# Kernel tuning notes

Hardware: AMD Instinct MI355X
Metric: run time of the kernel (lower is better)

Reference implementation:

```python
import jax, jax.numpy as jnp
from jax import lax
import numpy as np
import math

A = 9          # anchors per location
NC = 80        # classes
SCORE_T = 0.05
NMS_T = 0.5
DPI = 100      # detections_per_img (also per-level K in _inference)
BBOX_CLIP = math.log(1000.0 / 16.0)
LEVEL_SHAPES = [(64, 64), (32, 32), (16, 16), (8, 8)]
STRIDES = [8, 16, 32, 64]
BASE_SIZES = [32, 64, 128, 256]


def _conv(x, w, b):
    y = lax.conv_general_dilated(x, w, (1, 1), 'SAME', dimension_numbers=('NCHW', 'OIHW', 'NCHW'))
    return y + b[None, :, None, None]


def _head(feats, tower_w, tower_b, out_w, out_b, out_dim):
    outs = []
    for f in feats:
        x = f
        for i in range(tower_w.shape[0]):
            x = jax.nn.relu(_conv(x, tower_w[i], tower_b[i]))
        x = _conv(x, out_w, out_b)                     # [B, A*out_dim, H, W]
        B, _, H, W = x.shape
        x = x.reshape(B, A, out_dim, H, W).transpose(0, 3, 4, 1, 2).reshape(B, H * W * A, out_dim)
        outs.append(x)
    return outs


def _clip_boxes(b, img_h, img_w):
    x1 = jnp.clip(b[:, 0], 0.0, float(img_w)); y1 = jnp.clip(b[:, 1], 0.0, float(img_h))
    x2 = jnp.clip(b[:, 2], 0.0, float(img_w)); y2 = jnp.clip(b[:, 3], 0.0, float(img_h))
    return jnp.stack([x1, y1, x2, y2], axis=-1)


def _level_anchors(H, W, stride, s, img_h, img_w):
    # torchvision AnchorGenerator: sizes (s, s*2^(1/3), s*2^(2/3)), ratios (0.5,1,2)
    sizes = jnp.array([s, int(s * 2 ** (1 / 3)), int(s * 2 ** (2 / 3))], dtype=jnp.float32)
    ratios = jnp.array([0.5, 1.0, 2.0], dtype=jnp.float32)
    h_r = jnp.sqrt(ratios); w_r = 1.0 / h_r
    ws = (w_r[:, None] * sizes[None, :]).reshape(-1)
    hs = (h_r[:, None] * sizes[None, :]).reshape(-1)
    base = jnp.round(jnp.stack([-ws, -hs, ws, hs], axis=-1) / 2.0)   # [9,4]
    sx = (jnp.arange(W) * stride).astype(jnp.float32)
    sy = (jnp.arange(H) * stride).astype(jnp.float32)
    yy, xx = jnp.meshgrid(sy, sx, indexing='ij')
    shifts = jnp.stack([xx, yy, xx, yy], axis=-1).reshape(-1, 1, 4)   # [H*W,1,4]
    anch = (shifts + base[None]).reshape(-1, 4)                        # [H*W*A,4]
    return _clip_boxes(anch, img_h, img_w)


def _decode(rel, anch):
    # BoxCoder.decode_single with weights (1,1,1,1)
    w = anch[:, 2] - anch[:, 0]; h = anch[:, 3] - anch[:, 1]
    cx = anch[:, 0] + 0.5 * w;   cy = anch[:, 1] + 0.5 * h
    dx, dy = rel[:, 0], rel[:, 1]
    dw = jnp.minimum(rel[:, 2], BBOX_CLIP)
    dh = jnp.minimum(rel[:, 3], BBOX_CLIP)
    pcx = dx * w + cx; pcy = dy * h + cy
    pw = jnp.exp(dw) * w; ph = jnp.exp(dh) * h
    return jnp.stack([pcx - 0.5 * pw, pcy - 0.5 * ph, pcx + 0.5 * pw, pcy + 0.5 * ph], axis=-1)


def _pairwise_iou(boxes):
    area = (boxes[:, 2] - boxes[:, 0]) * (boxes[:, 3] - boxes[:, 1])
    lt = jnp.maximum(boxes[:, None, :2], boxes[None, :, :2])
    rb = jnp.minimum(boxes[:, None, 2:], boxes[None, :, 2:])
    wh = jnp.clip(rb - lt, 0.0)
    inter = wh[..., 0] * wh[..., 1]
    return inter / (area[:, None] + area[None, :] - inter + 1e-9)


def _per_image(logits, regs, anchors, img_h, img_w):
    bs, ss, ls = [], [], []
    for logit, reg, anch in zip(logits, regs, anchors):
        scores = jax.nn.sigmoid(logit).reshape(-1)                   # [N*NC]
        masked = jnp.where(scores > SCORE_T, scores, -1.0)
        top_s, idx = lax.top_k(masked, DPI)                          # fixed K = detections_per_img
        aidx = idx // NC
        lbl = idx % NC
        boxes = _clip_boxes(_decode(reg[aidx], anch[aidx]), img_h, img_w)
        valid = top_s > SCORE_T
        bs.append(boxes)
        ss.append(jnp.where(valid, top_s, -1.0))
        ls.append(jnp.where(valid, lbl, -1))
    boxes = jnp.concatenate(bs, 0); scores = jnp.concatenate(ss, 0); labels = jnp.concatenate(ls, 0)
    # batched (per-class) NMS via label coordinate offsets
    order = jnp.argsort(-scores)
    boxes_s = boxes[order]; scores_s = scores[order]; labels_s = labels[order]
    offset = labels_s.astype(boxes.dtype) * (float(max(img_h, img_w)) + 1.0)
    iou = lax.stop_gradient(_pairwise_iou(boxes_s + offset[:, None]))
    N = scores_s.shape[0]
    ar = jnp.arange(N)
    def body(i, keep):
        sup = keep[i] & (iou[i] > NMS_T) & (ar > i)
        return keep & ~sup
    keep = lax.fori_loop(0, N, body, scores_s > SCORE_T)
    fs, fi = lax.top_k(jnp.where(keep, scores_s, -1.0), DPI)
    ok = fs > SCORE_T
    fb = jnp.where(ok[:, None], boxes_s[fi], 0.0)
    fl = jnp.where(ok, labels_s[fi], -1)
    fs = jnp.where(ok, fs, 0.0)
    return fb, fs, fl


def setup_inputs() -> dict:
    key = jax.random.key(0)
    ks = jax.random.split(key, 8)
    B = 4
    w_scale = 0.04
    inp = {}
    shapes = [(B, 256, 64, 64), (B, 256, 32, 32), (B, 256, 16, 16), (B, 256, 8, 8)]
    for i, sh in enumerate(shapes):
        inp[f'f{i}'] = jax.random.normal(ks[i], sh, dtype=jnp.float32)
    inp['cls_tower_w'] = jax.random.normal(ks[4], (4, 256, 256, 3, 3), dtype=jnp.float32) * w_scale
    inp['cls_tower_b'] = jnp.zeros((4, 256), dtype=jnp.float32)
    inp['cls_out_w'] = jax.random.normal(ks[5], (A * NC, 256, 3, 3), dtype=jnp.float32) * w_scale
    inp['cls_out_b'] = jnp.full((A * NC,), -2.0, dtype=jnp.float32)  # prior-like bias
    inp['reg_tower_w'] = jax.random.normal(ks[6], (4, 256, 256, 3, 3), dtype=jnp.float32) * w_scale
    inp['reg_tower_b'] = jnp.zeros((4, 256), dtype=jnp.float32)
    inp['reg_out_w'] = jax.random.normal(ks[7], (A * 4, 256, 3, 3), dtype=jnp.float32) * w_scale
    inp['reg_out_b'] = jnp.zeros((A * 4,), dtype=jnp.float32)
    inp['image_h'] = 512
    inp['image_w'] = 512
    return inp


def reference(f0, f1, f2, f3, cls_tower_w, cls_tower_b, cls_out_w, cls_out_b,
              reg_tower_w, reg_tower_b, reg_out_w, reg_out_b, image_h, image_w):
    feats = [f0, f1, f2, f3]
    cls_logits = _head(feats, cls_tower_w, cls_tower_b, cls_out_w, cls_out_b, NC)   # list of [B,Ni,NC]
    bbox_regs = _head(feats, reg_tower_w, reg_tower_b, reg_out_w, reg_out_b, 4)     # list of [B,Ni,4]
    anchors = [_level_anchors(H, W, st, s, image_h, image_w)
               for (H, W), st, s in zip(LEVEL_SHAPES, STRIDES, BASE_SIZES)]
    fn = lambda ls, rs: _per_image(ls, rs, anchors, image_h, image_w)
    boxes, scores, labels = jax.vmap(fn)(tuple(cls_logits), tuple(bbox_regs))
    return boxes, scores, labels
```

## Files before the change

kernel.cpp:

```cpp
#include <hip/hip_runtime.h>
#include <math.h>

#define A_NUM 9
#define NCLS 80
#define IMG_KEY 3916800
#define IMG_REG 195840
#define CAP 8192
#define HBINS 16384

#define PCHUNK 12032
#define CHUNK_SLOTS 24064
#define CHUNK_BYTES (CHUNK_SLOTS * 16)
#define ACT_SLAB ((size_t)CHUNK_BYTES * 16)
#define WCHUNK_BYTES 40960
#define WCOG_BYTES (WCHUNK_BYTES * 16)

typedef _Float16 h8 __attribute__((ext_vector_type(8)));
typedef float fx4 __attribute__((ext_vector_type(4)));
typedef unsigned short u16;

__constant__ int   c_W[4]       = {64, 32, 16, 8};
__constant__ int   c_stride[4]  = {8, 16, 32, 64};
__constant__ float c_sizes[4][3]= {{32.f,40.f,50.f},{64.f,80.f,101.f},{128.f,161.f,203.f},{256.f,322.f,406.f}};
__constant__ int   c_keyOff[4]  = {0, 2949120, 3686400, 3870720};
__constant__ int   c_keyCnt[4]  = {2949120, 737280, 184320, 46080};
__constant__ int   c_regOff[4]  = {0, 147456, 184320, 193536};
__constant__ int   c_C[4]       = {66, 34, 18, 18};
__constant__ int   c_plvl[4]    = {0, 8712, 11024, 11672};
__constant__ int   c_pOff[4]    = {0, 1024, 1280, 1344};

__device__ __forceinline__ void gl_lds16(const void* g, void* l) {
    __builtin_amdgcn_global_load_lds(
        (const __attribute__((address_space(1))) void*)g,
        (__attribute__((address_space(3))) void*)l, 16, 0, 0);
}

__global__ __launch_bounds__(256) void pad16_k(
    const float* __restrict__ f0, const float* __restrict__ f1,
    const float* __restrict__ f2, const float* __restrict__ f3,
    char* __restrict__ Pin)
{
    int idx = blockIdx.x * 256 + threadIdx.x;
    const int PER_IMG = 16 * 2 * 1360;
    if (idx >= 4 * PER_IMG) return;
    int img = idx / PER_IMG;
    int r = idx - img * PER_IMG;
    int chunk = r / (2 * 1360);
    int r2 = r - chunk * (2 * 1360);
    int hfsel = r2 / 1360;
    int p = r2 - hfsel * 1360;
    int lvl = (p < 1024) ? 0 : (p < 1280 ? 1 : (p < 1344 ? 2 : 3));
    int u = p - c_pOff[lvl];
    int sh = 4 - lvl;
    int y = u >> sh;
    int xg = u & ((1 << sh) - 1);
    int x0 = xg * 4;
    int W = 64 >> lvl;
    const float* f = (lvl == 0) ? f0 : (lvl == 1) ? f1 : (lvl == 2) ? f2 : f3;
    int ci0 = chunk * 16 + hfsel * 8;
    float4 v[8];
    #pragma unroll
    for (int j = 0; j < 8; ++j)
        v[j] = *reinterpret_cast<const float4*>(
            f + ((size_t)(img * 256 + ci0 + j)) * (W * W) + y * W + x0);
    char* base = Pin + (size_t)img * ACT_SLAB + (size_t)chunk * CHUNK_BYTES;
    const int C = c_C[lvl];
    size_t rowSlot = (size_t)c_plvl[lvl] + (size_t)((y + 1) * 2 + hfsel) * C;
    #pragma unroll
    for (int c = 0; c < 4; ++c) {
        h8 hv, lv;
        #pragma unroll
        for (int j = 0; j < 8; ++j) {
            float val = (c == 0) ? v[j].x : (c == 1) ? v[j].y : (c == 2) ? v[j].z : v[j].w;
            _Float16 hh = (_Float16)val;
            hv[j] = hh;
            lv[j] = (_Float16)(val - (float)hh);
        }
        size_t slot = rowSlot + (x0 + c + 1);
        *reinterpret_cast<h8*>(base + slot * 16) = hv;
        *reinterpret_cast<h8*>(base + (slot + PCHUNK) * 16) = lv;
    }
}

__global__ __launch_bounds__(256) void repack16_k(
    const float* __restrict__ src, u16* __restrict__ dst,
    int C_out, int nCg, int total)
{
    int idx = blockIdx.x * 256 + threadIdx.x;
    if (idx >= total) return;
    int per = nCg * 16 * 1280;
    int layer = idx / per;
    int r = idx - layer * per;
    int cg = r / (16 * 1280);
    int r2 = r - cg * (16 * 1280);
    int chunk = r2 / 1280;
    int s = r2 - chunk * 1280;
    int co = s & 63;
    int r3 = s >> 6;
    int hfsel = r3 & 1;
    int kk = r3 >> 1;
    int coG = cg * 64 + co;
    float v[8];
    if (kk < 9 && coG < C_out) {
        const float* sp = src + ((size_t)(layer * C_out + coG)) * 2304
                        + (size_t)(chunk * 16 + hfsel * 8) * 9 + kk;
        #pragma unroll
        for (int j = 0; j < 8; ++j) v[j] = sp[j * 9];
    } else {
        #pragma unroll
        for (int j = 0; j < 8; ++j) v[j] = 0.f;
    }
    h8 hv, lv;
    #pragma unroll
    for (int j = 0; j < 8; ++j) {
        _Float16 hh = (_Float16)v[j];
        hv[j] = hh;
        lv[j] = (_Float16)(v[j] - (float)hh);
    }
    size_t e = ((size_t)((layer * nCg + cg) * 16 + chunk)) * 20480
             + (size_t)(kk >> 1) * 2048 + (size_t)(kk & 1) * 1024
             + (size_t)hfsel * 512 + (size_t)co * 8;
    *reinterpret_cast<h8*>(dst + e) = hv;
    *reinterpret_cast<h8*>(dst + e + 10240) = lv;
}

__global__ __launch_bounds__(256, 2) void conv16(
    const char* __restrict__ Pin, const char* __restrict__ bufIn, char* __restrict__ bufOut,
    const u16* __restrict__ repA, const float* __restrict__ bA,
    const u16* __restrict__ repB, const float* __restrict__ bB,
    unsigned* __restrict__ keys, float* __restrict__ regb,
    int mode, int usePin)
{
    const int tid = threadIdx.x;
    const int lane = tid & 63;
    const int wv = tid >> 6;

    int img, head, coBase, C_out, epi, tile;
    if (mode == 0) {
        int hw = blockIdx.x;
        int logical = (hw & 7) * 88 + (hw >> 3);
        int z = logical / 88;
        int rem = logical - z * 88;
        tile = rem >> 2;
        coBase = (rem & 3) * 64;
        img = z & 3; head = z >> 2;
        C_out = 256; epi = 0;
    } else {
        int hw = blockIdx.x;
        int logical = (hw & 7) * 143 + (hw >> 3);
        img = logical / 286;
        int rem = logical - img * 286;
        tile = rem / 13;
        int yy = rem - tile * 13;
        if (yy < 12) { head = 0; coBase = yy * 64; C_out = 720; epi = 1; }
        else         { head = 1; coBase = 0;       C_out = 36;  epi = 2; }
    }
    const float* bsel = head ? bB : bA;
    const u16* wsel = head ? repB : repA;
    const char* wBase = (const char*)wsel + (size_t)(coBase >> 6) * WCOG_BYTES;

    int lvl, ty, tx;
    if (tile < 16)      { lvl = 0; ty = tile >> 2; tx = tile & 3; }
    else if (tile < 20) { int u = tile - 16; lvl = 1; ty = u >> 1; tx = u & 1; }
    else if (tile == 20){ lvl = 2; ty = 0; tx = 0; }
    else                { lvl = 3; ty = 0; tx = 0; }
    const int W = 64 >> lvl;
    const int C = c_C[lvl];
    const int plvl = c_plvl[lvl];
    const int tileY = ty * 16, tileX = tx * 16;

    const char* srcB = usePin ? Pin + (size_t)img * ACT_SLAB
                              : bufIn + (size_t)(head * 4 + img) * ACT_SLAB;

    __shared__ alignas(16) char sA[2][10368];
    __shared__ alignas(16) char sB[2][20480];

    const int laneCol = lane & 15;
    const int g = lane >> 4;
    const int halfS = g & 1;
    const int tapS = g >> 1;
    const int laneBv = tapS * 2048 + halfS * 1024 + laneCol * 16;
    int laneAhi[5];
    int AloOff[5];
    #pragma unroll
    for (int k = 0; k < 5; ++k) {
        int kk = 2 * k + tapS; if (kk > 8) kk = 8;
        int ky = kk / 3;
        int kx = kk - ky * 3;
        laneAhi[k] = ky * 576 + halfS * 288 + (laneCol + kx) * 16;
        AloOff[k] = PCHUNK * 16
                  + (plvl + ((tileY + wv * 4 + ky) * 2 + halfS) * C
                     + tileX + laneCol + kx) * 16;
    }
    const int mtStride = 2 * C * 16;

    int aByte[3]; bool aOk[3];
    #pragma unroll
    for (int p = 0; p < 3; ++p) {
        int s = tid + 256 * p;
        aOk[p] = (s < 648);
        int sc = aOk[p] ? s : 647;
        int row = sc / 36;
        int q = sc - row * 36;
        int hf = q / 18;
        int col = q - hf * 18;
        aByte[p] = (plvl + ((tileY + row) * 2 + hf) * C + tileX + col) * 16;
    }

    fx4 acc[4][4];
    #pragma unroll
    for (int mt = 0; mt < 4; ++mt)
        #pragma unroll
        for (int nt = 0; nt < 4; ++nt)
            acc[mt][nt] = (fx4){0.f, 0.f, 0.f, 0.f};

    {
        const char* srcCk = srcB;
        const char* wCk = wBase;
        #pragma unroll
        for (int p = 0; p < 3; ++p)
            if (aOk[p]) gl_lds16(srcCk + aByte[p], (char*)sA[0] + (wv * 64 + 256 * p) * 16);
        for (int j = wv; j < 20; j += 4)
            gl_lds16(wCk + j * 1024 + lane * 16, (char*)sB[0] + j * 1024);
    }
    asm volatile("s_waitcnt vmcnt(0)" ::: "memory");
    __builtin_amdgcn_s_barrier();

    #pragma unroll 1
    for (int ck = 0; ck < 16; ++ck) {
        const int cur = ck & 1;
        const char* srcCk = srcB + (size_t)ck * CHUNK_BYTES;
        const char* wLo = wBase + (size_t)ck * WCHUNK_BYTES + 20480;

        h8 Bl[2][4], Al[2][4];
        #pragma unroll
        for (int nt = 0; nt < 4; ++nt)
            Bl[0][nt] = *reinterpret_cast<const h8*>(wLo + laneBv + nt * 256);
        #pragma unroll
        for (int mt = 0; mt < 4; ++mt)
            Al[0][mt] = *reinterpret_cast<const h8*>(srcCk + AloOff[0] + mt * mtStride);

        if (ck < 15) {
            const char* srcN = srcB + (size_t)(ck + 1) * CHUNK_BYTES;
            const char* wN = wBase + (size_t)(ck + 1) * WCHUNK_BYTES;
            #pragma unroll
            for (int p = 0; p < 3; ++p)
                if (aOk[p]) gl_lds16(srcN + aByte[p], (char*)sA[cur ^ 1] + (wv * 64 + 256 * p) * 16);
            for (int j = wv; j < 20; j += 4)
                gl_lds16(wN + j * 1024 + lane * 16, (char*)sB[cur ^ 1] + j * 1024);
        }

        #pragma unroll
        for (int k = 0; k < 5; ++k) {
            const int sl = k & 1;
            if (k < 4) {
                const char* wlk = wLo + (k + 1) * 4096;
                #pragma unroll
                for (int nt = 0; nt < 4; ++nt)
                    Bl[sl ^ 1][nt] = *reinterpret_cast<const h8*>(wlk + laneBv + nt * 256);
                #pragma unroll
                for (int mt = 0; mt < 4; ++mt)
                    Al[sl ^ 1][mt] = *reinterpret_cast<const h8*>(srcCk + AloOff[k + 1] + mt * mtStride);
            }
            const char* bk = sB[cur] + k * 4096;
            h8 Bh[4];
            #pragma unroll
            for (int nt = 0; nt < 4; ++nt)
                Bh[nt] = *reinterpret_cast<const h8*>(bk + laneBv + nt * 256);
            #pragma unroll
            for (int mt = 0; mt < 4; ++mt) {
                h8 Ah = *reinterpret_cast<const h8*>(sA[cur] + (wv * 4 + mt) * 576 + laneAhi[k]);
                #pragma unroll
                for (int nt = 0; nt < 4; ++nt) {
                    acc[mt][nt] = __builtin_amdgcn_mfma_f32_16x16x32_f16(Ah, Bh[nt], acc[mt][nt], 0, 0, 0);
                    acc[mt][nt] = __builtin_amdgcn_mfma_f32_16x16x32_f16(Ah, Bl[sl][nt], acc[mt][nt], 0, 0, 0);
                    acc[mt][nt] = __builtin_amdgcn_mfma_f32_16x16x32_f16(Al[sl][mt], Bh[nt], acc[mt][nt], 0, 0, 0);
                }
            }
        }

        asm volatile("s_waitcnt vmcnt(0)" ::: "memory");
        __builtin_amdgcn_sched_barrier(0);
        __builtin_amdgcn_s_barrier();
    }

    const int HW = W * W;
    if (epi == 0) {
        char* dstB = bufOut + (size_t)(head * 4 + img) * ACT_SLAB;
        _Float16* eW = reinterpret_cast<_Float16*>((char*)sB[0] + wv * 1024);
        const int ci8 = laneCol & 7;
        const int hf  = laneCol >> 3;
        const int rpx = lane & 15, rhalf = (lane >> 4) & 1, rplane = lane >> 5;
        const int rOff = rpx * 32 + rplane * 16 + rhalf * 8;
        const int rx = tileX + rpx;
        #pragma unroll
        for (int mt = 0; mt < 4; ++mt) {
            int y = tileY + wv * 4 + mt;
            bool yok = (y < W);
            #pragma unroll
            for (int nt = 0; nt < 4; ++nt) {
                int coG = coBase + nt * 16 + laneCol;
                float b = bsel[coG];
                #pragma unroll
                for (int i = 0; i < 4; ++i) {
                    float v = fmaxf(acc[mt][nt][i] + b, 0.f);
                    _Float16 hh = (_Float16)v;
                    _Float16 ll = (_Float16)(v - (float)hh);
                    int px = g * 4 + i;
                    eW[px * 32 + hf * 8 + ci8] = hh;
                    eW[px * 32 + 16 + hf * 8 + ci8] = ll;
                }
                __syncthreads();
                if (yok && rx < W) {
                    int chunkIdx = (coBase + nt * 16) >> 4;
                    size_t slot = (size_t)chunkIdx * CHUNK_SLOTS + (size_t)rplane * PCHUNK
                                + plvl + (size_t)((y + 1) * 2 + rhalf) * C + (rx + 1);
                    *reinterpret_cast<h8*>(dstB + slot * 16) =
                        *reinterpret_cast<const h8*>(eW + rOff);
                }
                __syncthreads();
            }
        }
    } else if (epi == 1) {
        unsigned* kb = keys + (size_t)img * IMG_KEY + c_keyOff[lvl];
        #pragma unroll
        for (int mt = 0; mt < 4; ++mt) {
            int y = tileY + wv * 4 + mt;
            int x0 = tileX + g * 4;
            if (y >= W || x0 >= W) continue;
            #pragma unroll
            for (int nt = 0; nt < 4; ++nt) {
                int coG = coBase + nt * 16 + laneCol;
                if (coG >= C_out) continue;
                float b = bsel[coG];
                unsigned kq[4];
                #pragma unroll
                for (int i = 0; i < 4; ++i) {
                    float sc = 1.0f / (1.0f + expf(-(acc[mt][nt][i] + b)));
                    kq[i] = (sc > 0.05f) ? __float_as_uint(sc) : 0u;
                }
                *reinterpret_cast<uint4*>(kb + (size_t)coG * HW + y * W + x0) =
                    make_uint4(kq[0], kq[1], kq[2], kq[3]);
            }
        }
    } else {
        float* rb = regb + (size_t)img * IMG_REG + c_regOff[lvl];
        #pragma unroll
        for (int mt = 0; mt < 4; ++mt) {
            int y = tileY + wv * 4 + mt;
            if (y >= W) continue;
            #pragma unroll
            for (int nt = 0; nt < 4; ++nt) {
                int coG = nt * 16 + laneCol;
                if (coG >= C_out) continue;
                float b = bsel[coG];
                int a = coG >> 2, jj = coG & 3;
                #pragma unroll
                for (int i = 0; i < 4; ++i) {
                    int x = tileX + g * 4 + i;
                    if (x >= W) continue;
                    rb[((size_t)(y * W + x) * A_NUM + a) * 4 + jj] = acc[mt][nt][i] + b;
                }
            }
        }
    }
}

__global__ __launch_bounds__(256) void hist_k(const unsigned* __restrict__ keys,
                                              unsigned* __restrict__ hist)
{
    int il = blockIdx.y, img = il >> 2, lvl = il & 3;
    int n = c_keyCnt[lvl];
    int chunk = blockIdx.x * 16384;
    if (chunk >= n) return;
    __shared__ unsigned h[HBINS];
    for (int t = threadIdx.x; t < HBINS; t += 256) h[t] = 0;
    __syncthreads();
    const uint4* k4 = (const uint4*)(keys + (size_t)img * IMG_KEY + c_keyOff[lvl]);
    int i0 = chunk >> 2, i1 = min(chunk + 16384, n) >> 2;
    for (int i = i0 + (int)threadIdx.x; i < i1; i += 256) {
        uint4 kv = k4[i];
        if (kv.x) atomicAdd(&h[kv.x >> 18], 1u);
        if (kv.y) atomicAdd(&h[kv.y >> 18], 1u);
        if (kv.z) atomicAdd(&h[kv.z >> 18], 1u);
        if (kv.w) atomicAdd(&h[kv.w >> 18], 1u);
    }
    __syncthreads();
    unsigned* gh = hist + (size_t)il * HBINS;
    for (int t = threadIdx.x; t < HBINS; t += 256)
        if (h[t]) atomicAdd(&gh[t], h[t]);
}

__global__ __launch_bounds__(256) void thresh_k(const unsigned* __restrict__ hist,
                                                unsigned* __restrict__ tbin)
{
    const unsigned* h = hist + (size_t)blockIdx.x * HBINS;
    __shared__ unsigned cs[256];
    int tid = threadIdx.x;
    unsigned s = 0;
    int base = tid * 64;
    for (int q = 0; q < 64; ++q) { int b = base + q; if (b >= 1) s += h[b]; }
    cs[tid] = s;
    __syncthreads();
    if (tid == 0) {
        unsigned total = 0, sel = 0;
        for (int c = 255; c >= 0; --c) {
            if (total + cs[c] >= 100u) {
                int lo = (c == 0) ? 1 : c * 64;
                for (int b = c * 64 + 63; b >= lo; --b) {
                    total += h[b];
                    if (total >= 100u) { sel = (unsigned)b; break; }
                }
                break;
            }
            total += cs[c];
        }
        tbin[blockIdx.x] = sel;
    }
}

__global__ __launch_bounds__(256) void compact_k(const unsigned* __restrict__ keys,
                                                 const unsigned* __restrict__ tbin,
                                                 unsigned* __restrict__ cnt,
                                                 uint2* __restrict__ comp)
{
    int il = blockIdx.y, img = il >> 2, lvl = il & 3;
    int n = c_keyCnt[lvl];
    int chunk = blockIdx.x * 16384;
    if (chunk >= n) return;
    const uint4* k4 = (const uint4*)(keys + (size_t)img * IMG_KEY + c_keyOff[lvl]);
    unsigned thr = tbin[il] << 18;
    int shift = 12 - 2 * lvl;
    int hwm = (1 << shift) - 1;
    int i0 = chunk >> 2, i1 = min(chunk + 16384, n) >> 2;
    __shared__ unsigned lcnt, lbase, lcur;
    if (threadIdx.x == 0) { lcnt = 0; lcur = 0; }
    __syncthreads();
    unsigned myc = 0;
    for (int i = i0 + (int)threadIdx.x; i < i1; i += 256) {
        uint4 kv = k4[i];
        myc += (kv.x != 0u && kv.x >= thr);
        myc += (kv.y != 0u && kv.y >= thr);
        myc += (kv.z != 0u && kv.z >= thr);
        myc += (kv.w != 0u && kv.w >= thr);
    }
    if (myc) atomicAdd(&lcnt, myc);
    __syncthreads();
    if (threadIdx.x == 0 && lcnt) lbase = atomicAdd(&cnt[il], lcnt);
    __syncthreads();
    if (lcnt == 0) return;
    uint2* c = comp + (size_t)il * CAP;
    for (int i = i0 + (int)threadIdx.x; i < i1; i += 256) {
        uint4 kv = k4[i];
        unsigned kk[4] = {kv.x, kv.y, kv.z, kv.w};
        #pragma unroll
        for (int j = 0; j < 4; ++j) {
            unsigned key = kk[j];
            if (key != 0u && key >= thr) {
                int t = i * 4 + j;
                int co = t >> shift, p = t & hwm;
                int a = co / NCLS, cls = co - a * NCLS;
                unsigned idx = (unsigned)((p * A_NUM + a) * NCLS + cls);
                unsigned pos = lbase + atomicAdd(&lcur, 1u);
                if (pos < CAP) c[pos] = make_uint2(key, idx);
            }
        }
    }
}

__global__ __launch_bounds__(256) void topsort_k(const unsigned* __restrict__ cnt,
                                                 const uint2* __restrict__ comp,
                                                 uint2* __restrict__ topk)
{
    __shared__ unsigned long long s[CAP];
    int il = blockIdx.x, tid = threadIdx.x;
    int n = (int)min(cnt[il], (unsigned)CAP);
    const uint2* c = comp + (size_t)il * CAP;
    for (int i = tid; i < CAP; i += 256) {
        unsigned long long v = 0ull;
        if (i < n) {
            uint2 e = c[i];
            v = ((unsigned long long)e.x << 32) | (unsigned long long)(~e.y);
        }
        s[i] = v;
    }
    for (int k = 2; k <= CAP; k <<= 1) {
        for (int j = k >> 1; j > 0; j >>= 1) {
            __syncthreads();
            for (int p = tid; p < CAP / 2; p += 256) {
                int i = ((p & ~(j - 1)) << 1) | (p & (j - 1));
                int ixj = i | j;
                unsigned long long a = s[i], b = s[ixj];
                if (((i & k) == 0) ? (a < b) : (a > b)) { s[i] = b; s[ixj] = a; }
            }
        }
    }
    __syncthreads();
    if (tid < 100) {
        unsigned long long v = s[tid];
        topk[il * 100 + tid] = make_uint2((unsigned)(v >> 32), ~(unsigned)(v & 0xFFFFFFFFull));
    }
}

__global__ void decode_k(const uint2* __restrict__ topk, const float* __restrict__ regb,
                         float* __restrict__ cboxes, float* __restrict__ cscores,
                         int* __restrict__ clabels, const int* __restrict__ ph, const int* __restrict__ pw)
{
    int il = blockIdx.x, img = il >> 2, lvl = il & 3;
    int j = threadIdx.x;
    if (j >= 100) return;
    float imgW = (float)pw[0], imgH = (float)ph[0];
    uint2 tk = topk[il * 100 + j];
    int outP = img * 400 + lvl * 100 + j;
    if (tk.x == 0u) {
        cboxes[outP * 4 + 0] = 0.f; cboxes[outP * 4 + 1] = 0.f;
        cboxes[outP * 4 + 2] = 0.f; cboxes[outP * 4 + 3] = 0.f;
        cscores[outP] = -1.0f; clabels[outP] = -1;
        return;
    }
    float score = __uint_as_float(tk.x);
    unsigned idx = tk.y;
    int aidx = (int)(idx / NCLS);
    int lbl  = (int)(idx - (unsigned)aidx * NCLS);
    int a = aidx % A_NUM, p = aidx / A_NUM;
    int W = c_W[lvl];
    int y = p / W, x = p - y * W;
    int r = a / 3, si = a - r * 3;
    float ratio = (r == 0) ? 0.5f : ((r == 1) ? 1.0f : 2.0f);
    float size = c_sizes[lvl][si];
    float hr = sqrtf(ratio);
    float wr = 1.0f / hr;
    float wsz = wr * size, hsz = hr * size;
    float bw = rintf(wsz * 0.5f), bh = rintf(hsz * 0.5f);
    float sx = (float)(x * c_stride[lvl]), sy = (float)(y * c_stride[lvl]);
    float ax1 = fminf(fmaxf(sx - bw, 0.f), imgW);
    float ay1 = fminf(fmaxf(sy - bh, 0.f), imgH);
    float ax2 = fminf(fmaxf(sx + bw, 0.f), imgW);
    float ay2 = fminf(fmaxf(sy + bh, 0.f), imgH);
    float aw = ax2 - ax1, ah = ay2 - ay1;
    float cx = ax1 + 0.5f * aw, cy = ay1 + 0.5f * ah;
    const float* rel = regb + (size_t)img * IMG_REG + c_regOff[lvl] + (size_t)aidx * 4;
    float dx = rel[0], dy = rel[1];
    float dw = fminf(rel[2], 4.135166556742356f);
    float dh = fminf(rel[3], 4.135166556742356f);
    float pcx = dx * aw + cx, pcy = dy * ah + cy;
    float pwd = expf(dw) * aw, phd = expf(dh) * ah;
    float x1 = pcx - 0.5f * pwd, y1 = pcy - 0.5f * phd;
    float x2 = pcx + 0.5f * pwd, y2 = pcy + 0.5f * phd;
    cboxes[outP * 4 + 0] = fminf(fmaxf(x1, 0.f), imgW);
    cboxes[outP * 4 + 1] = fminf(fmaxf(y1, 0.f), imgH);
    cboxes[outP * 4 + 2] = fminf(fmaxf(x2, 0.f), imgW);
    cboxes[outP * 4 + 3] = fminf(fmaxf(y2, 0.f), imgH);
    cscores[outP] = score;
    clabels[outP] = lbl;
}

__global__ __launch_bounds__(512) void nms_k(const float* __restrict__ cboxes,
                                             const float* __restrict__ cscores,
                                             const int* __restrict__ clabels,
                                             const int* __restrict__ ph, const int* __restrict__ pw,
                                             float* __restrict__ out)
{
    int img = blockIdx.x, tid = threadIdx.x;
    __shared__ float sSc[512];
    __shared__ int   sPos[512];
    __shared__ float bx1[400], by1[400], bx2[400], by2[400], sAr[400];
    __shared__ int   sKeep[400], sLbl[400];
    float imgH = (float)ph[0], imgW = (float)pw[0];
    float offm = fmaxf(imgH, imgW) + 1.0f;

    sSc[tid] = (tid < 400) ? cscores[img * 400 + tid] : -3.0f;
    sPos[tid] = tid;
    __syncthreads();

    for (int k = 2; k <= 512; k <<= 1) {
        for (int jj = k >> 1; jj > 0; jj >>= 1) {
            int ixj = tid ^ jj;
            if (ixj > tid) {
                float s1 = sSc[tid], s2 = sSc[ixj];
                int p1 = sPos[tid], p2 = sPos[ixj];
                bool bef = (s1 > s2) || (s1 == s2 && p1 < p2);
                bool sw = ((tid & k) == 0) ? (!bef) : bef;
                if (sw) { sSc[tid] = s2; sSc[ixj] = s1; sPos[tid] = p2; sPos[ixj] = p1; }
            }
            __syncthreads();
        }
    }

    if (tid < 400) {
        int p = sPos[tid];
        int lbl = clabels[img * 400 + p];
        float ofs = (float)lbl * offm;
        float x1 = cboxes[(img * 400 + p) * 4 + 0] + ofs;
        float y1 = cboxes[(img * 400 + p) * 4 + 1] + ofs;
        float x2 = cboxes[(img * 400 + p) * 4 + 2] + ofs;
        float y2 = cboxes[(img * 400 + p) * 4 + 3] + ofs;
        bx1[tid] = x1; by1[tid] = y1; bx2[tid] = x2; by2[tid] = y2;
        sAr[tid] = (x2 - x1) * (y2 - y1);
        sLbl[tid] = lbl;
        sKeep[tid] = (sSc[tid] > 0.05f) ? 1 : 0;
    }
    __syncthreads();

    for (int i = 0; i < 400; ++i) {
        if (sKeep[i]) {
            for (int j2 = i + 1 + tid; j2 < 400; j2 += 512) {
                float ltx = fmaxf(bx1[i], bx1[j2]), lty = fmaxf(by1[i], by1[j2]);
                float rbx = fminf(bx2[i], bx2[j2]), rby = fminf(by2[i], by2[j2]);
                float ww = fmaxf(rbx - ltx, 0.f), hh = fmaxf(rby - lty, 0.f);
                float inter = ww * hh;
                float iou = inter / (((sAr[i] + sAr[j2]) - inter) + 1e-9f);
                if (iou > 0.5f) sKeep[j2] = 0;
            }
        }
        __syncthreads();
    }

    if (tid == 0) {
        int rank = 0;
        for (int i = 0; i < 400 && rank < 100; ++i) {
            if (sKeep[i]) {
                int p = sPos[i];
                for (int kk = 0; kk < 4; ++kk)
                    out[(img * 100 + rank) * 4 + kk] = cboxes[(img * 400 + p) * 4 + kk];
                out[1600 + img * 100 + rank] = sSc[i];
                out[2000 + img * 100 + rank] = (float)sLbl[i];
                ++rank;
            }
        }
        for (; rank < 100; ++rank) {
            for (int kk = 0; kk < 4; ++kk) out[(img * 100 + rank) * 4 + kk] = 0.f;
            out[1600 + img * 100 + rank] = 0.f;
            out[2000 + img * 100 + rank] = -1.0f;
        }
    }
}

extern "C" void kernel_launch(void* const* d_in, const int* in_sizes, int n_in,
                              void* d_out, int out_size, void* d_ws, size_t ws_size,
                              hipStream_t stream)
{
    const float* f0 = (const float*)d_in[0];
    const float* f1 = (const float*)d_in[1];
    const float* f2 = (const float*)d_in[2];
    const float* f3 = (const float*)d_in[3];
    const float* cls_tw = (const float*)d_in[4];
    const float* cls_tb = (const float*)d_in[5];
    const float* cls_ow = (const float*)d_in[6];
    const float* cls_ob = (const float*)d_in[7];
    const float* reg_tw = (const float*)d_in[8];
    const float* reg_tb = (const float*)d_in[9];
    const float* reg_ow = (const float*)d_in[10];
    const float* reg_ob = (const float*)d_in[11];
    const int* ph = (const int*)d_in[12];
    const int* pw = (const int*)d_in[13];
    float* out = (float*)d_out;

    char* ws = (char*)d_ws;
    size_t off = 0;
    auto alloc = [&](size_t bytes) -> void* {
        void* p = ws + off;
        off = (off + bytes + 1023) & ~(size_t)1023;
        return p;
    };
    const size_t KEYS = (size_t)4 * IMG_KEY * 4;
    const size_t ACT8 = ACT_SLAB * 8;
    char*     Pin    = (char*)alloc(ACT_SLAB * 4 + 32768);
    char*     slabA  = (char*)alloc((KEYS > ACT8 ? KEYS : ACT8) + 32768);
    unsigned* keys   = (unsigned*)slabA;
    char*     actA   = slabA;
    char*     actB   = (char*)alloc(ACT8 + 32768);
    u16*      repCT  = (u16*)alloc((size_t)16 * WCOG_BYTES);
    u16*      repRT  = (u16*)alloc((size_t)16 * WCOG_BYTES);
    u16*      repCO  = (u16*)alloc((size_t)12 * WCOG_BYTES);
    u16*      repRO  = (u16*)alloc((size_t)1 * WCOG_BYTES);
    float*    regb   = (float*)alloc((size_t)4 * IMG_REG * 4);
    unsigned* hist   = (unsigned*)alloc((size_t)16 * HBINS * 4);
    unsigned* cnt    = (unsigned*)alloc(16 * 4);
    unsigned* tbin   = (unsigned*)alloc(16 * 4);
    uint2*    comp   = (uint2*)alloc((size_t)16 * CAP * 8);
    uint2*    topk   = (uint2*)alloc((size_t)1600 * 8);
    float*    cboxes = (float*)alloc((size_t)4 * 400 * 4 * 4);
    float*    cscores= (float*)alloc((size_t)4 * 400 * 4);
    int*      clabels= (int*)alloc((size_t)4 * 400 * 4);

    hipMemsetAsync(Pin, 0, ACT_SLAB * 4, stream);
    hipMemsetAsync(actA, 0, ACT8, stream);
    hipMemsetAsync(actB, 0, ACT8, stream);
    hipMemsetAsync(hist, 0, (size_t)16 * HBINS * 4, stream);
    hipMemsetAsync(cnt, 0, 64, stream);

    {
        int tPad = 4 * 16 * 2 * 1360;
        pad16_k<<<(tPad + 255) / 256, 256, 0, stream>>>(f0, f1, f2, f3, Pin);
        int tT = 4 * 4 * 16 * 1280;
        repack16_k<<<(tT + 255) / 256, 256, 0, stream>>>(cls_tw, repCT, 256, 4, tT);
        repack16_k<<<(tT + 255) / 256, 256, 0, stream>>>(reg_tw, repRT, 256, 4, tT);
        int tCO = 12 * 16 * 1280;
        repack16_k<<<(tCO + 255) / 256, 256, 0, stream>>>(cls_ow, repCO, 720, 12, tCO);
        int tRO = 16 * 1280;
        repack16_k<<<(tRO + 255) / 256, 256, 0, stream>>>(reg_ow, repRO, 36, 1, tRO);
    }

    const size_t RL = (size_t)4 * 16 * 20480;
    conv16<<<704, 256, 0, stream>>>(Pin, Pin, actA,
        repCT, cls_tb, repRT, reg_tb, keys, regb, 0, 1);
    conv16<<<704, 256, 0, stream>>>(Pin, actA, actB,
        repCT + RL, cls_tb + 256, repRT + RL, reg_tb + 256, keys, regb, 0, 0);
    conv16<<<704, 256, 0, stream>>>(Pin, actB, actA,
        repCT + 2 * RL, cls_tb + 512, repRT + 2 * RL, reg_tb + 512, keys, regb, 0, 0);
    conv16<<<704, 256, 0, stream>>>(Pin, actA, actB,
        repCT + 3 * RL, cls_tb + 768, repRT + 3 * RL, reg_tb + 768, keys, regb, 0, 0);
    conv16<<<1144, 256, 0, stream>>>(Pin, actB, nullptr,
        repCO, cls_ob, repRO, reg_ob, keys, regb, 1, 0);

    hist_k<<<dim3(180, 16), 256, 0, stream>>>(keys, hist);
    thresh_k<<<16, 256, 0, stream>>>(hist, tbin);
    compact_k<<<dim3(180, 16), 256, 0, stream>>>(keys, tbin, cnt, comp);
    topsort_k<<<16, 256, 0, stream>>>(cnt, comp, topk);
    decode_k<<<16, 128, 0, stream>>>(topk, regb, cboxes, cscores, clabels, ph, pw);
    nms_k<<<4, 512, 0, stream>>>(cboxes, cscores, clabels, ph, pw, out);
}
```

Measured before the change: 1.398 ms.

## Stage low-half fp16 operands in LDS instead of reading them from global

The conv kernel used to stage only the high-half fp16 activations and weights in LDS and read the low-half correction terms straight from global memory through per-lane loads. Both halves are now staged in doubled LDS buffers, and the three MFMA passes (hi*hi, hi*lo, lo*hi) run as separate loops over register tiles loaded from LDS. LDS use roughly doubles to about 123KB per block, so launch bounds drop to one block per CU, which cuts occupancy and the latency hiding it gave. The hand-written waitcnt/barrier pair is replaced with __syncthreads, and workspace padding grows to cover the larger over-reads.

```diff
diff --git a/kernel.cpp b/kernel.cpp
--- a/kernel.cpp
+++ b/kernel.cpp
@@ -124,7 +124,7 @@
     *reinterpret_cast<h8*>(dst + e + 10240) = lv;
 }
 
-__global__ __launch_bounds__(256, 2) void conv16(
+__global__ __launch_bounds__(256, 1) void conv16(
     const char* __restrict__ Pin, const char* __restrict__ bufIn, char* __restrict__ bufOut,
     const u16* __restrict__ repA, const float* __restrict__ bA,
     const u16* __restrict__ repB, const float* __restrict__ bB,
@@ -172,8 +172,8 @@
     const char* srcB = usePin ? Pin + (size_t)img * ACT_SLAB
                               : bufIn + (size_t)(head * 4 + img) * ACT_SLAB;
 
-    __shared__ alignas(16) char sA[2][10368];
-    __shared__ alignas(16) char sB[2][20480];
+    __shared__ alignas(16) char sA[2][20736];
+    __shared__ alignas(16) char sB[2][40960];
 
     const int laneCol = lane & 15;
     const int g = lane >> 4;
@@ -181,30 +181,27 @@
     const int tapS = g >> 1;
     const int laneBv = tapS * 2048 + halfS * 1024 + laneCol * 16;
     int laneAhi[5];
-    int AloOff[5];
     #pragma unroll
     for (int k = 0; k < 5; ++k) {
         int kk = 2 * k + tapS; if (kk > 8) kk = 8;
         int ky = kk / 3;
         int kx = kk - ky * 3;
-        laneAhi[k] = ky * 576 + halfS * 288 + (laneCol + kx) * 16;
-        AloOff[k] = PCHUNK * 16
-                  + (plvl + ((tileY + wv * 4 + ky) * 2 + halfS) * C
-                     + tileX + laneCol + kx) * 16;
-    }
-    const int mtStride = 2 * C * 16;
-
-    int aByte[3]; bool aOk[3];
+        laneAhi[k] = ky * 1152 + halfS * 288 + (laneCol + kx) * 16;
+    }
+
+    int aByte[6]; bool aOk[6];
     #pragma unroll
-    for (int p = 0; p < 3; ++p) {
+    for (int p = 0; p < 6; ++p) {
         int s = tid + 256 * p;
-        aOk[p] = (s < 648);
-        int sc = aOk[p] ? s : 647;
-        int row = sc / 36;
-        int q = sc - row * 36;
-        int hf = q / 18;
-        int col = q - hf * 18;
-        aByte[p] = (plvl + ((tileY + row) * 2 + hf) * C + tileX + col) * 16;
+        aOk[p] = (s < 1296);
+        int sc = aOk[p] ? s : 1295;
+        int row = sc / 72;
+        int q = sc - row * 72;
+        int pl = q / 36;
+        int q2 = q - pl * 36;
+        int hf = q2 / 18;
+        int col = q2 - hf * 18;
+        aByte[p] = (plvl + pl * PCHUNK + ((tileY + row) * 2 + hf) * C + tileX + col) * 16;
     }
 
     fx4 acc[4][4];
@@ -218,70 +215,61 @@
         const char* srcCk = srcB;
         const char* wCk = wBase;
         #pragma unroll
-        for (int p = 0; p < 3; ++p)
+        for (int p = 0; p < 6; ++p)
             if (aOk[p]) gl_lds16(srcCk + aByte[p], (char*)sA[0] + (wv * 64 + 256 * p) * 16);
-        for (int j = wv; j < 20; j += 4)
+        for (int j = wv; j < 40; j += 4)
             gl_lds16(wCk + j * 1024 + lane * 16, (char*)sB[0] + j * 1024);
     }
-    asm volatile("s_waitcnt vmcnt(0)" ::: "memory");
-    __builtin_amdgcn_s_barrier();
+    __syncthreads();
 
     #pragma unroll 1
     for (int ck = 0; ck < 16; ++ck) {
         const int cur = ck & 1;
-        const char* srcCk = srcB + (size_t)ck * CHUNK_BYTES;
-        const char* wLo = wBase + (size_t)ck * WCHUNK_BYTES + 20480;
-
-        h8 Bl[2][4], Al[2][4];
-        #pragma unroll
-        for (int nt = 0; nt < 4; ++nt)
-            Bl[0][nt] = *reinterpret_cast<const h8*>(wLo + laneBv + nt * 256);
-        #pragma unroll
-        for (int mt = 0; mt < 4; ++mt)
-            Al[0][mt] = *reinterpret_cast<const h8*>(srcCk + AloOff[0] + mt * mtStride);
 
         if (ck < 15) {
             const char* srcN = srcB + (size_t)(ck + 1) * CHUNK_BYTES;
             const char* wN = wBase + (size_t)(ck + 1) * WCHUNK_BYTES;
             #pragma unroll
-            for (int p = 0; p < 3; ++p)
+            for (int p = 0; p < 6; ++p)
                 if (aOk[p]) gl_lds16(srcN + aByte[p], (char*)sA[cur ^ 1] + (wv * 64 + 256 * p) * 16);
-            for (int j = wv; j < 20; j += 4)
+            for (int j = wv; j < 40; j += 4)
                 gl_lds16(wN + j * 1024 + lane * 16, (char*)sB[cur ^ 1] + j * 1024);
         }
 
         #pragma unroll
         for (int k = 0; k < 5; ++k) {
-            const int sl = k & 1;
-            if (k < 4) {
-                const char* wlk = wLo + (k + 1) * 4096;
+            const char* bk = sB[cur] + k * 4096;
+            h8 Bh[4], Bl[4];
+            #pragma unroll
+            for (int nt = 0; nt < 4; ++nt) {
+                Bh[nt] = *reinterpret_cast<const h8*>(bk + laneBv + nt * 256);
+                Bl[nt] = *reinterpret_cast<const h8*>(bk + 20480 + laneBv + nt * 256);
+            }
+            h8 Ah[4], Al[4];
+            #pragma unroll
+            for (int mt = 0; mt < 4; ++mt) {
+                const char* am = sA[cur] + (wv * 4 + mt) * 1152 + laneAhi[k];
+                Ah[mt] = *reinterpret_cast<const h8*>(am);
+                Al[mt] = *reinterpret_cast<const h8*>(am + 576);
+            }
+            #pragma unroll
+            for (int mt = 0; mt < 4; ++mt)
                 #pragma unroll
                 for (int nt = 0; nt < 4; ++nt)
-                    Bl[sl ^ 1][nt] = *reinterpret_cast<const h8*>(wlk + laneBv + nt * 256);
+                    acc[mt][nt] = __builtin_amdgcn_mfma_f32_16x16x32_f16(Ah[mt], Bh[nt], acc[mt][nt], 0, 0, 0);
+            #pragma unroll
+            for (int mt = 0; mt < 4; ++mt)
                 #pragma unroll
-                for (int mt = 0; mt < 4; ++mt)
-                    Al[sl ^ 1][mt] = *reinterpret_cast<const h8*>(srcCk + AloOff[k + 1] + mt * mtStride);
-            }
-            const char* bk = sB[cur] + k * 4096;
-            h8 Bh[4];
-            #pragma unroll
-            for (int nt = 0; nt < 4; ++nt)
-                Bh[nt] = *reinterpret_cast<const h8*>(bk + laneBv + nt * 256);
-            #pragma unroll
-            for (int mt = 0; mt < 4; ++mt) {
-                h8 Ah = *reinterpret_cast<const h8*>(sA[cur] + (wv * 4 + mt) * 576 + laneAhi[k]);
+                for (int nt = 0; nt < 4; ++nt)
+                    acc[mt][nt] = __builtin_amdgcn_mfma_f32_16x16x32_f16(Ah[mt], Bl[nt], acc[mt][nt], 0, 0, 0);
+            #pragma unroll
+            for (int mt = 0; mt < 4; ++mt)
                 #pragma unroll
-                for (int nt = 0; nt < 4; ++nt) {
-                    acc[mt][nt] = __builtin_amdgcn_mfma_f32_16x16x32_f16(Ah, Bh[nt], acc[mt][nt], 0, 0, 0);
-                    acc[mt][nt] = __builtin_amdgcn_mfma_f32_16x16x32_f16(Ah, Bl[sl][nt], acc[mt][nt], 0, 0, 0);
-                    acc[mt][nt] = __builtin_amdgcn_mfma_f32_16x16x32_f16(Al[sl][mt], Bh[nt], acc[mt][nt], 0, 0, 0);
-                }
-            }
-        }
-
-        asm volatile("s_waitcnt vmcnt(0)" ::: "memory");
-        __builtin_amdgcn_sched_barrier(0);
-        __builtin_amdgcn_s_barrier();
+                for (int nt = 0; nt < 4; ++nt)
+                    acc[mt][nt] = __builtin_amdgcn_mfma_f32_16x16x32_f16(Al[mt], Bh[nt], acc[mt][nt], 0, 0, 0);
+        }
+
+        __syncthreads();
     }
 
     const int HW = W * W;
@@ -665,11 +653,11 @@
     };
     const size_t KEYS = (size_t)4 * IMG_KEY * 4;
     const size_t ACT8 = ACT_SLAB * 8;
-    char*     Pin    = (char*)alloc(ACT_SLAB * 4 + 32768);
-    char*     slabA  = (char*)alloc((KEYS > ACT8 ? KEYS : ACT8) + 32768);
+    char*     Pin    = (char*)alloc(ACT_SLAB * 4 + 65536);
+    char*     slabA  = (char*)alloc((KEYS > ACT8 ? KEYS : ACT8) + 65536);
     unsigned* keys   = (unsigned*)slabA;
     char*     actA   = slabA;
-    char*     actB   = (char*)alloc(ACT8 + 32768);
+    char*     actB   = (char*)alloc(ACT8 + 65536);
     u16*      repCT  = (u16*)alloc((size_t)16 * WCOG_BYTES);
     u16*      repRT  = (u16*)alloc((size_t)16 * WCOG_BYTES);
     u16*      repCO  = (u16*)alloc((size_t)12 * WCOG_BYTES);
```

Result: slower. 1.489 ms (+6.5%).
